# Kernel optimization log

Measured on AMD Instinct MI355X. Metric: run time of the kernel, lower is better.

The kernel has to match this reference:

```python
import jax, jax.numpy as jnp
import numpy as np

EMBED_DIM = 64
NUM_GROUPS = 16
KEY_DIM = 64
WAVE_LENGTH = 1000.0


def setup_inputs() -> dict:
    key = jax.random.key(0)
    ks = jax.random.split(key, 8)
    N, R, D = 4, 512, 1024
    features = jax.random.normal(ks[0], (N, R, D), dtype=jnp.float32)
    # valid boxes: ymin/xmin in [0,800), heights/widths in [1,201)
    u = jax.random.uniform(ks[1], (N, R, 4), dtype=jnp.float32)
    ymin = u[..., 0] * 800.0
    xmin = u[..., 1] * 800.0
    ymax = ymin + 1.0 + u[..., 2] * 200.0
    xmax = xmin + 1.0 + u[..., 3] * 200.0
    boxes = jnp.stack([ymin, xmin, ymax, xmax], axis=-1)  # [N,R,4]
    s = 0.02
    geo_w = jax.random.normal(ks[2], (EMBED_DIM, NUM_GROUPS), dtype=jnp.float32) * s
    geo_b = jnp.zeros((NUM_GROUPS,), dtype=jnp.float32)
    Wq = jax.random.normal(ks[3], (D, KEY_DIM), dtype=jnp.float32) * s
    bq = jnp.zeros((KEY_DIM,), dtype=jnp.float32)
    Wk = jax.random.normal(ks[4], (D, KEY_DIM), dtype=jnp.float32) * s
    bk = jnp.zeros((KEY_DIM,), dtype=jnp.float32)
    Wv = jax.random.normal(ks[5], (D, D // NUM_GROUPS), dtype=jnp.float32) * s
    bv = jnp.zeros((D // NUM_GROUPS,), dtype=jnp.float32)
    return {"features": features, "boxes": boxes, "geo_w": geo_w, "geo_b": geo_b,
            "Wq": Wq, "bq": bq, "Wk": Wk, "bk": bk, "Wv": Wv, "bv": bv}


def _geometry_embeddings(boxes):
    # boxes: [N,R,4] -> embeddings [N,R,R,EMBED_DIM]
    ymin, xmin, ymax, xmax = jnp.split(boxes, 4, axis=2)  # each [N,R,1]
    height = ymax - ymin + 1.0
    width = xmax - xmin + 1.0
    cy = 0.5 * (ymin + ymax)
    cx = 0.5 * (xmin + xmax)
    cyT = jnp.transpose(cy, (0, 2, 1))
    cxT = jnp.transpose(cx, (0, 2, 1))
    dy = jnp.log(jnp.maximum((cy - cyT) / height, 1e-5))          # [N,R,R]
    dx = jnp.log(jnp.maximum((cx - cxT) / width, 1e-5))
    dh = jnp.log(height / jnp.transpose(height, (0, 2, 1)))
    dw = jnp.log(width / jnp.transpose(width, (0, 2, 1)))
    pos = jnp.stack([dy, dx, dh, dw], axis=3)                     # [N,R,R,4]
    feat_range = jnp.arange(EMBED_DIM // 8, dtype=jnp.float32)
    dim_mat = jnp.power(WAVE_LENGTH, (8.0 / EMBED_DIM) * feat_range)  # [8]
    div = (100.0 * pos)[..., None] / dim_mat                      # [N,R,R,4,8]
    emb = jnp.concatenate([jnp.sin(div), jnp.cos(div)], axis=4)   # [N,R,R,4,16]
    N, R = boxes.shape[0], boxes.shape[1]
    return emb.reshape(N, R, R, EMBED_DIM)


def reference(features, boxes, geo_w, geo_b, Wq, bq, Wk, bk, Wv, bv):
    N, R, D = features.shape
    G = NUM_GROUPS
    dk = KEY_DIM // G  # per-group key dim
    emb = _geometry_embeddings(boxes)                              # [N,R,R,E]
    # 1x1 conv + relu over pairwise embedding channels
    geometry_weight = jax.nn.relu(jnp.einsum('nqke,eg->nqkg', emb, geo_w) + geo_b)
    geometry_weight = jnp.transpose(geometry_weight, (0, 1, 3, 2))  # [N,R,G,R]
    q = (features @ Wq + bq).reshape(N, R, G, dk)
    k = (features @ Wk + bk).reshape(N, R, G, dk)
    v = features @ Wv + bv                                          # [N,R,D/G]
    dot = jnp.einsum('nqgd,nkgd->ngqk', q, k) / jnp.sqrt(jnp.float32(dk))
    appearance_weight = jnp.transpose(dot, (0, 2, 1, 3))            # [N,R,G,R]
    relation = jnp.log(jnp.maximum(geometry_weight, 1e-6)) + appearance_weight
    relation = jax.nn.softmax(relation, axis=3)                     # [N,R,G,R]
    out = jnp.einsum('nqgk,nkv->nqgv', relation, v)                 # [N,R,G,D/G]
    out = out.reshape(N, R, D)
    return features + out
```

## Files before the change

kernel.cpp:

```cpp
#include <hip/hip_runtime.h>
#include <stdint.h>

#define R_ 512
#define D_ 1024
#define G_ 16
#define NT 256

typedef __attribute__((ext_vector_type(8))) short short8;
typedef __attribute__((ext_vector_type(4))) float floatx4;

__device__ __forceinline__ unsigned pk2bf(float a, float b) {
    unsigned ua = __builtin_bit_cast(unsigned, a) + 0x8000u;
    unsigned ub = __builtin_bit_cast(unsigned, b) + 0x8000u;
    return (ub & 0xFFFF0000u) | (ua >> 16);
}
__device__ __forceinline__ unsigned short f2bf(float a) {
    return (unsigned short)((__builtin_bit_cast(unsigned, a) + 0x8000u) >> 16);
}

__global__ __launch_bounds__(256) void prep_kernel(
    const float* __restrict__ Wq, const float* __restrict__ Wk,
    const float* __restrict__ Wv, const float* __restrict__ geo_w,
    const float* __restrict__ boxes,
    unsigned short* __restrict__ WTb, unsigned short* __restrict__ geoF,
    float4* __restrict__ bp4, float2* __restrict__ bp2, int NR)
{
    const int b = blockIdx.x, t = threadIdx.x;
    if (b < 48) {
        __shared__ float s[64][65];
        const int mat = b >> 4, rblk = b & 15;
        const float* Wsrc = (mat == 0) ? Wq : (mat == 1) ? Wk : Wv;
        const int d0 = rblk * 64;
        #pragma unroll
        for (int i = 0; i < 16; i++) {
            int e = t + i * 256;
            s[e >> 6][e & 63] = Wsrc[(size_t)(d0 + (e >> 6)) * 64 + (e & 63)];
        }
        __syncthreads();
        #pragma unroll
        for (int i = 0; i < 16; i++) {
            int e = t + i * 256;
            int c = e >> 6, r = e & 63;
            WTb[(size_t)(mat * 64 + c) * 1024 + d0 + r] = f2bf(s[r][c]);
        }
    } else if (b == 48) {
        #pragma unroll
        for (int i = 0; i < 4; i++) {
            int idx = t * 4 + i;
            int h = idx >> 9, rem = idx & 511, ll = rem >> 3, j = rem & 7;
            int e = h * 32 + (ll >> 4) * 8 + j, cc = ll & 15;
            geoF[idx] = f2bf(geo_w[e * G_ + cc]);
        }
    } else {
        int r = (b - 49) * 256 + t;
        if (r < NR) {
            float ymin = boxes[r*4+0], xmin = boxes[r*4+1];
            float ymax = boxes[r*4+2], xmax = boxes[r*4+3];
            float h = ymax - ymin + 1.0f, w = xmax - xmin + 1.0f;
            bp4[r] = make_float4(0.5f * (ymin + ymax), 0.5f * (xmin + xmax),
                                 __logf(h), __logf(w));
            bp2[r] = make_float2(1.0f / h, 1.0f / w);
        }
    }
}

__global__ __launch_bounds__(256) void proj_kernel(
    const float* __restrict__ feat, const unsigned short* __restrict__ WTb,
    const float* __restrict__ bq, const float* __restrict__ bk,
    const float* __restrict__ bv,
    unsigned short* __restrict__ qd16, unsigned short* __restrict__ kb16,
    unsigned short* __restrict__ vT16)
{
    __shared__ __align__(16) unsigned short s_A[16][1032];

    const int t = threadIdx.x, l = t & 63, w = t >> 6;
    const int mb = blockIdx.x / 3, ng = blockIdx.x % 3;
    const long row0 = (long)mb * 16;

    const float4* f4 = (const float4*)(feat + row0 * D_);
    #pragma unroll
    for (int i = 0; i < 16; i++) {
        int e = t + i * 256;
        int row = e >> 8, c4 = e & 255;
        float4 v = f4[e];
        uint2 pk;
        pk.x = pk2bf(v.x, v.y);
        pk.y = pk2bf(v.z, v.w);
        *(uint2*)&s_A[row][c4 * 4] = pk;
    }
    __syncthreads();

    const int lc = l & 15, q = l >> 4;
    const int gcol = (ng * 4 + w) * 16 + lc;
    const unsigned short* bptr = WTb + (size_t)gcol * 1024 + q * 8;

    floatx4 acc = {0.f, 0.f, 0.f, 0.f};
    #pragma unroll 8
    for (int k0 = 0; k0 < 1024; k0 += 32) {
        short8 a  = *(const short8*)&s_A[lc][k0 + q * 8];
        short8 bb = *(const short8*)(bptr + k0);
        acc = __builtin_amdgcn_mfma_f32_16x16x32_bf16(a, bb, acc, 0, 0, 0);
    }

    const int mat = gcol >> 6, mcol = gcol & 63;
    const float* B = (mat == 0) ? bq : (mat == 1) ? bk : bv;
    const float bias = B[mcol];
    #pragma unroll
    for (int r = 0; r < 4; r++) {
        long gr = row0 + q * 4 + r;
        float val = acc[r] + bias;
        if (mat == 0)      qd16[gr * 64 + mcol] = f2bf(0.5f * val);
        else if (mat == 1) kb16[gr * 64 + mcol] = f2bf(val);
        else               vT16[((size_t)((gr >> 9) * 64 + mcol)) * 512 + (gr & 511)] = f2bf(val);
    }
}

__global__ __launch_bounds__(256, 3) void relation_kernel(
    const float* __restrict__ feat, const float* __restrict__ geo_b,
    const unsigned short* __restrict__ geoF, const unsigned short* __restrict__ qd16,
    const unsigned short* __restrict__ kb16, const unsigned short* __restrict__ vT16,
    const float4* __restrict__ bp4, const float2* __restrict__ bp2,
    float* __restrict__ out)
{
    __shared__ __align__(16) unsigned short s_p[2][16][520];
    __shared__ float s_redm[2][4][16];
    __shared__ float s_reds[2][4][16];

    const int t = threadIdx.x;
    const int l = t & 63;
    const int w = t >> 6;
    const int c = l & 15;
    const int quad = l >> 4;
    const int nqA = blockIdx.x * 2, nqB = nqA + 1;
    const int n = nqA >> 9;

    const float4 qbA = bp4[nqA], qbB = bp4[nqB];
    const float2 qiA = bp2[nqA], qiB = bp2[nqB];
    const float gbias = geo_b[c];

    short8 bgeo0 = *(const short8*)(geoF + l * 8);
    short8 bgeo1 = *(const short8*)(geoF + 512 + l * 8);

    const bool act = (quad == ((c >> 1) & 3));
    const int hsel = c >> 3, jhalf = c & 1;
    uint2 qvA = *(const uint2*)(qd16 + (size_t)nqA * 64 + c * 4);
    uint2 qvB = *(const uint2*)(qd16 + (size_t)nqB * 64 + c * 4);
    short qA[4] = {(short)(qvA.x & 0xFFFF), (short)(qvA.x >> 16),
                   (short)(qvA.y & 0xFFFF), (short)(qvA.y >> 16)};
    short qB[4] = {(short)(qvB.x & 0xFFFF), (short)(qvB.x >> 16),
                   (short)(qvB.y & 0xFFFF), (short)(qvB.y >> 16)};
    short8 bqfA0, bqfA1, bqfB0, bqfB1;
    #pragma unroll
    for (int j = 0; j < 8; j++) {
        bool on0 = act && (hsel == 0) && ((j >> 2) == jhalf);
        bool on1 = act && (hsel == 1) && ((j >> 2) == jhalf);
        bqfA0[j] = on0 ? qA[j & 3] : (short)0;
        bqfA1[j] = on1 ? qA[j & 3] : (short)0;
        bqfB0[j] = on0 ? qB[j & 3] : (short)0;
        bqfB1[j] = on1 ? qB[j & 3] : (short)0;
    }

    const float C8[8] = {
        15.91549431f,
        15.91549431f * 0.4216965034f,
        15.91549431f * 0.1778279410f,
        15.91549431f * 0.0749894209f,
        15.91549431f * 0.0316227766f,
        15.91549431f * 0.0133352143f,
        15.91549431f * 0.0056234133f,
        15.91549431f * 0.0023713737f };

    const float offs = (quad & 1) ? 0.25f : 0.0f;
    const bool qlow = (quad < 2);

    float logitA[8][4], logitB[8][4];
    const int krow0 = n * R_ + w * 128;

    #pragma unroll
    for (int ti = 0; ti < 8; ti++) {
        float4 kb = bp4[krow0 + ti * 16 + c];

        float aA  = qlow ? (qbA.x - kb.x) * qiA.x : (qbA.y - kb.y) * qiA.y;
        float pAa = __logf(fmaxf(aA, 1e-5f));
        float pAb = qlow ? (qbA.z - kb.z) : (qbA.w - kb.w);
        float aB  = qlow ? (qbB.x - kb.x) * qiB.x : (qbB.y - kb.y) * qiB.y;
        float pBa = __logf(fmaxf(aB, 1e-5f));
        float pBb = qlow ? (qbB.z - kb.z) : (qbB.w - kb.w);

        short8 aeA0, aeA1, aeB0, aeB1;
        #pragma unroll
        for (int j = 0; j < 8; j++) {
            float r;
            r = pAa * C8[j]; r = r - rintf(r) + offs;
            aeA0[j] = (short)f2bf(__builtin_amdgcn_sinf(r));
            r = pAb * C8[j]; r = r - rintf(r) + offs;
            aeA1[j] = (short)f2bf(__builtin_amdgcn_sinf(r));
            r = pBa * C8[j]; r = r - rintf(r) + offs;
            aeB0[j] = (short)f2bf(__builtin_amdgcn_sinf(r));
            r = pBb * C8[j]; r = r - rintf(r) + offs;
            aeB1[j] = (short)f2bf(__builtin_amdgcn_sinf(r));
        }

        const unsigned short* kr = kb16 + (size_t)(krow0 + ti * 16 + c) * 64;
        short8 ak0 = *(const short8*)(kr + quad * 8);
        short8 ak1 = *(const short8*)(kr + 32 + quad * 8);

        floatx4 accgA = {0,0,0,0}, acckA = {0,0,0,0};
        floatx4 accgB = {0,0,0,0}, acckB = {0,0,0,0};
        accgA = __builtin_amdgcn_mfma_f32_16x16x32_bf16(aeA0, bgeo0, accgA, 0, 0, 0);
        accgA = __builtin_amdgcn_mfma_f32_16x16x32_bf16(aeA1, bgeo1, accgA, 0, 0, 0);
        accgB = __builtin_amdgcn_mfma_f32_16x16x32_bf16(aeB0, bgeo0, accgB, 0, 0, 0);
        accgB = __builtin_amdgcn_mfma_f32_16x16x32_bf16(aeB1, bgeo1, accgB, 0, 0, 0);
        acckA = __builtin_amdgcn_mfma_f32_16x16x32_bf16(ak0, bqfA0, acckA, 0, 0, 0);
        acckA = __builtin_amdgcn_mfma_f32_16x16x32_bf16(ak1, bqfA1, acckA, 0, 0, 0);
        acckB = __builtin_amdgcn_mfma_f32_16x16x32_bf16(ak0, bqfB0, acckB, 0, 0, 0);
        acckB = __builtin_amdgcn_mfma_f32_16x16x32_bf16(ak1, bqfB1, acckB, 0, 0, 0);

        #pragma unroll
        for (int r = 0; r < 4; r++) {
            logitA[ti][r] = __logf(fmaxf(accgA[r] + gbias, 1e-6f)) + acckA[r];
            logitB[ti][r] = __logf(fmaxf(accgB[r] + gbias, 1e-6f)) + acckB[r];
        }
    }

    float mxA = -3.0e38f, mxB = -3.0e38f;
    #pragma unroll
    for (int ti = 0; ti < 8; ti++)
        #pragma unroll
        for (int r = 0; r < 4; r++) {
            mxA = fmaxf(mxA, logitA[ti][r]);
            mxB = fmaxf(mxB, logitB[ti][r]);
        }
    mxA = fmaxf(mxA, __shfl_xor(mxA, 16));
    mxA = fmaxf(mxA, __shfl_xor(mxA, 32));
    mxB = fmaxf(mxB, __shfl_xor(mxB, 16));
    mxB = fmaxf(mxB, __shfl_xor(mxB, 32));
    if (l < 16) { s_redm[0][w][l] = mxA; s_redm[1][w][l] = mxB; }
    __syncthreads();
    float mgA = fmaxf(fmaxf(s_redm[0][0][c], s_redm[0][1][c]),
                      fmaxf(s_redm[0][2][c], s_redm[0][3][c]));
    float mgB = fmaxf(fmaxf(s_redm[1][0][c], s_redm[1][1][c]),
                      fmaxf(s_redm[1][2][c], s_redm[1][3][c]));

    float sumA = 0.f, sumB = 0.f;
    #pragma unroll
    for (int ti = 0; ti < 8; ti++) {
        int k0 = w * 128 + ti * 16 + quad * 4;
        float eA0 = __expf(logitA[ti][0] - mgA);
        float eA1 = __expf(logitA[ti][1] - mgA);
        float eA2 = __expf(logitA[ti][2] - mgA);
        float eA3 = __expf(logitA[ti][3] - mgA);
        sumA += (eA0 + eA1) + (eA2 + eA3);
        uint2 pkA; pkA.x = pk2bf(eA0, eA1); pkA.y = pk2bf(eA2, eA3);
        *(uint2*)&s_p[0][c][k0] = pkA;
        float eB0 = __expf(logitB[ti][0] - mgB);
        float eB1 = __expf(logitB[ti][1] - mgB);
        float eB2 = __expf(logitB[ti][2] - mgB);
        float eB3 = __expf(logitB[ti][3] - mgB);
        sumB += (eB0 + eB1) + (eB2 + eB3);
        uint2 pkB; pkB.x = pk2bf(eB0, eB1); pkB.y = pk2bf(eB2, eB3);
        *(uint2*)&s_p[1][c][k0] = pkB;
    }
    sumA += __shfl_xor(sumA, 16);
    sumA += __shfl_xor(sumA, 32);
    sumB += __shfl_xor(sumB, 16);
    sumB += __shfl_xor(sumB, 32);
    if (l < 16) { s_reds[0][w][l] = sumA; s_reds[1][w][l] = sumB; }
    __syncthreads();

    floatx4 accpA = {0,0,0,0}, accpB = {0,0,0,0};
    const unsigned short* vrow = vT16 + ((size_t)(n * 64 + w * 16 + c)) * 512;
    #pragma unroll
    for (int ks = 0; ks < 16; ks++) {
        short8 bv8 = *(const short8*)(vrow + ks * 32 + quad * 8);
        short8 apA = *(const short8*)(&s_p[0][c][ks * 32 + quad * 8]);
        short8 apB = *(const short8*)(&s_p[1][c][ks * 32 + quad * 8]);
        accpA = __builtin_amdgcn_mfma_f32_16x16x32_bf16(apA, bv8, accpA, 0, 0, 0);
        accpB = __builtin_amdgcn_mfma_f32_16x16x32_bf16(apB, bv8, accpB, 0, 0, 0);
    }

    #pragma unroll
    for (int r = 0; r < 4; r++) {
        int gg = quad * 4 + r;
        float sA = (s_reds[0][0][gg] + s_reds[0][1][gg]) + (s_reds[0][2][gg] + s_reds[0][3][gg]);
        float sB = (s_reds[1][0][gg] + s_reds[1][1][gg]) + (s_reds[1][2][gg] + s_reds[1][3][gg]);
        size_t oA = (size_t)nqA * D_ + (size_t)gg * 64 + w * 16 + c;
        size_t oB = (size_t)nqB * D_ + (size_t)gg * 64 + w * 16 + c;
        out[oA] = feat[oA] + accpA[r] / sA;
        out[oB] = feat[oB] + accpB[r] / sB;
    }
}

extern "C" void kernel_launch(void* const* d_in, const int* in_sizes, int n_in,
                              void* d_out, int out_size, void* d_ws, size_t ws_size,
                              hipStream_t stream) {
    const float* feat  = (const float*)d_in[0];
    const float* boxes = (const float*)d_in[1];
    const float* geo_w = (const float*)d_in[2];
    const float* geo_b = (const float*)d_in[3];
    const float* Wq    = (const float*)d_in[4];
    const float* bq    = (const float*)d_in[5];
    const float* Wk    = (const float*)d_in[6];
    const float* bk    = (const float*)d_in[7];
    const float* Wv    = (const float*)d_in[8];
    const float* bv    = (const float*)d_in[9];
    float* out = (float*)d_out;

    const int N  = in_sizes[0] / (R_ * D_);
    const int NR = N * R_;

    float4* bp4 = (float4*)d_ws;
    float2* bp2 = (float2*)(bp4 + NR);
    unsigned short* kb16 = (unsigned short*)(bp2 + NR);
    unsigned short* vT16 = kb16 + (size_t)NR * 64;
    unsigned short* qd16 = vT16 + (size_t)NR * 64;
    unsigned short* WTb  = qd16 + (size_t)NR * 64;
    unsigned short* geoF = WTb + (size_t)192 * 1024;

    prep_kernel<<<dim3(49 + (NR + 255) / 256), dim3(NT), 0, stream>>>(
        Wq, Wk, Wv, geo_w, boxes, WTb, geoF, bp4, bp2, NR);
    proj_kernel<<<dim3((NR / 16) * 3), dim3(NT), 0, stream>>>(
        feat, WTb, bq, bk, bv, qd16, kb16, vT16);
    relation_kernel<<<dim3(NR / 2), dim3(NT), 0, stream>>>(
        feat, geo_b, geoF, qd16, kb16, vT16, bp4, bp2, out);
}
```

Measured before the change: 56.34 us.

## Fuse softmax into logit loop by dropping max pass and log-exp pair

Rewrites the relation weights as relu(geometry) * exp(dot), which cancels the log of the geometry weight against the softmax exp. The softmax is no longer shifted by its maximum. This removes the per-element log, the max reduction, one block barrier, the shared max buffer and the 64-float logit register arrays, so the exp/pack/store now runs inside the first tile loop. Launch bounds are raised to 4 blocks per CU to use the freed registers. Without the max shift, large dot products could overflow exp, so correctness now depends on logits staying in a safe range.

New measurement: 50.90 us. 9.7% less time.

```diff
diff --git a/kernel.cpp b/kernel.cpp
--- a/kernel.cpp
+++ b/kernel.cpp
@@ -115,7 +115,7 @@
     }
 }
 
-__global__ __launch_bounds__(256, 3) void relation_kernel(
+__global__ __launch_bounds__(256, 4) void relation_kernel(
     const float* __restrict__ feat, const float* __restrict__ geo_b,
     const unsigned short* __restrict__ geoF, const unsigned short* __restrict__ qd16,
     const unsigned short* __restrict__ kb16, const unsigned short* __restrict__ vT16,
@@ -123,7 +123,6 @@
     float* __restrict__ out)
 {
     __shared__ __align__(16) unsigned short s_p[2][16][520];
-    __shared__ float s_redm[2][4][16];
     __shared__ float s_reds[2][4][16];
 
     const int t = threadIdx.x;
@@ -173,7 +172,7 @@
     const float offs = (quad & 1) ? 0.25f : 0.0f;
     const bool qlow = (quad < 2);
 
-    float logitA[8][4], logitB[8][4];
+    float sumA = 0.f, sumB = 0.f;
     const int krow0 = n * R_ + w * 128;
 
     #pragma unroll
@@ -216,51 +215,24 @@
         acckB = __builtin_amdgcn_mfma_f32_16x16x32_bf16(ak0, bqfB0, acckB, 0, 0, 0);
         acckB = __builtin_amdgcn_mfma_f32_16x16x32_bf16(ak1, bqfB1, acckB, 0, 0, 0);
 
-        #pragma unroll
-        for (int r = 0; r < 4; r++) {
-            logitA[ti][r] = __logf(fmaxf(accgA[r] + gbias, 1e-6f)) + acckA[r];
-            logitB[ti][r] = __logf(fmaxf(accgB[r] + gbias, 1e-6f)) + acckB[r];
-        }
-    }
-
-    float mxA = -3.0e38f, mxB = -3.0e38f;
-    #pragma unroll
-    for (int ti = 0; ti < 8; ti++)
-        #pragma unroll
-        for (int r = 0; r < 4; r++) {
-            mxA = fmaxf(mxA, logitA[ti][r]);
-            mxB = fmaxf(mxB, logitB[ti][r]);
-        }
-    mxA = fmaxf(mxA, __shfl_xor(mxA, 16));
-    mxA = fmaxf(mxA, __shfl_xor(mxA, 32));
-    mxB = fmaxf(mxB, __shfl_xor(mxB, 16));
-    mxB = fmaxf(mxB, __shfl_xor(mxB, 32));
-    if (l < 16) { s_redm[0][w][l] = mxA; s_redm[1][w][l] = mxB; }
-    __syncthreads();
-    float mgA = fmaxf(fmaxf(s_redm[0][0][c], s_redm[0][1][c]),
-                      fmaxf(s_redm[0][2][c], s_redm[0][3][c]));
-    float mgB = fmaxf(fmaxf(s_redm[1][0][c], s_redm[1][1][c]),
-                      fmaxf(s_redm[1][2][c], s_redm[1][3][c]));
-
-    float sumA = 0.f, sumB = 0.f;
-    #pragma unroll
-    for (int ti = 0; ti < 8; ti++) {
         int k0 = w * 128 + ti * 16 + quad * 4;
-        float eA0 = __expf(logitA[ti][0] - mgA);
-        float eA1 = __expf(logitA[ti][1] - mgA);
-        float eA2 = __expf(logitA[ti][2] - mgA);
-        float eA3 = __expf(logitA[ti][3] - mgA);
+        float eA0 = fmaxf(accgA[0] + gbias, 1e-6f) * __expf(acckA[0]);
+        float eA1 = fmaxf(accgA[1] + gbias, 1e-6f) * __expf(acckA[1]);
+        float eA2 = fmaxf(accgA[2] + gbias, 1e-6f) * __expf(acckA[2]);
+        float eA3 = fmaxf(accgA[3] + gbias, 1e-6f) * __expf(acckA[3]);
         sumA += (eA0 + eA1) + (eA2 + eA3);
         uint2 pkA; pkA.x = pk2bf(eA0, eA1); pkA.y = pk2bf(eA2, eA3);
         *(uint2*)&s_p[0][c][k0] = pkA;
-        float eB0 = __expf(logitB[ti][0] - mgB);
-        float eB1 = __expf(logitB[ti][1] - mgB);
-        float eB2 = __expf(logitB[ti][2] - mgB);
-        float eB3 = __expf(logitB[ti][3] - mgB);
+
+        float eB0 = fmaxf(accgB[0] + gbias, 1e-6f) * __expf(acckB[0]);
+        float eB1 = fmaxf(accgB[1] + gbias, 1e-6f) * __expf(acckB[1]);
+        float eB2 = fmaxf(accgB[2] + gbias, 1e-6f) * __expf(acckB[2]);
+        float eB3 = fmaxf(accgB[3] + gbias, 1e-6f) * __expf(acckB[3]);
         sumB += (eB0 + eB1) + (eB2 + eB3);
         uint2 pkB; pkB.x = pk2bf(eB0, eB1); pkB.y = pk2bf(eB2, eB3);
         *(uint2*)&s_p[1][c][k0] = pkB;
     }
+
     sumA += __shfl_xor(sumA, 16);
     sumA += __shfl_xor(sumA, 32);
     sumB += __shfl_xor(sumB, 16);
```
